# Performance work log

Hardware: AMD Instinct MI355X
Metric: run time of the kernel (lower is better)

The kernel has to match this reference:

```python
import jax, jax.numpy as jnp
import numpy as np


def setup_inputs() -> dict:
    key = jax.random.key(0)
    k1, k2, k3, k4 = jax.random.split(key, 4)
    B, S, H, P = 8, 2048, 1024, 4096
    hidden_states = jax.random.normal(k1, (B, S, H), dtype=jnp.float32)
    pairs = jax.random.randint(k2, (B, P, 2), 0, S, dtype=jnp.int64)
    # classifier params: Linear(2H -> H), Linear(H -> 2). Stored as (in, out).
    W1 = jax.random.normal(k3, (2 * H, H), dtype=jnp.float32) * (1.0 / np.sqrt(2 * H))
    b1 = jnp.zeros((H,), dtype=jnp.float32)
    W2 = jax.random.normal(k4, (H, 2), dtype=jnp.float32) * (1.0 / np.sqrt(H))
    b2 = jnp.zeros((2,), dtype=jnp.float32)
    return {"hidden_states": hidden_states, "pairs": pairs,
            "W1": W1, "b1": b1, "W2": W2, "b2": b2}


def reference(hidden_states, pairs, W1, b1, W2, b2):
    # Gather pair embeddings: (B, P, H) each.
    emb1 = jnp.take_along_axis(hidden_states, pairs[:, :, 0:1], axis=1)
    emb2 = jnp.take_along_axis(hidden_states, pairs[:, :, 1:2], axis=1)
    pair_emb = jnp.concatenate([emb1, emb2], axis=-1)  # (B, P, 2H)
    h = jnp.einsum('bpi,ih->bph', pair_emb, W1) + b1
    h = jax.nn.gelu(h, approximate=False)  # torch nn.GELU default is exact erf
    # Dropout is identity at inference.
    logits = jnp.einsum('bph,ho->bpo', h, W2) + b2  # (B, P, 2)
    return logits
```

## Files before the change

kernel.cpp:

```cpp
#include <hip/hip_runtime.h>
#include <hip/hip_bf16.h>

#define B_  8
#define S_  2048
#define H_  1024
#define P_  4096
#define K_  2048
#define M_  32768
#define NT_ 32

typedef unsigned short u16;
using bf16x8 = __attribute__((ext_vector_type(8))) short;
using f32x4  = __attribute__((ext_vector_type(4))) float;

#define AS1 __attribute__((address_space(1)))
#define AS3 __attribute__((address_space(3)))

__device__ inline u16 f2bf(float f) {
  union { float f; unsigned u; } c; c.f = f;
  unsigned u = c.u;
  unsigned r = (u + 0x7fffu + ((u >> 16) & 1u)) >> 16;
  return (u16)r;
}

__global__ void cvt_hidden_k(const float4* __restrict__ src,
                             ushort4* __restrict__ dst, int n4) {
  int i = blockIdx.x * blockDim.x + threadIdx.x;
  int stride = gridDim.x * blockDim.x;
  for (; i < n4; i += stride) {
    float4 v = src[i];
    ushort4 o;
    o.x = f2bf(v.x); o.y = f2bf(v.y); o.z = f2bf(v.z); o.w = f2bf(v.w);
    dst[i] = o;
  }
}

__global__ void transp_w1_k(const float* __restrict__ w1, u16* __restrict__ w1t) {
  __shared__ float tile[32][33];
  int n0 = blockIdx.x * 32;
  int k0 = blockIdx.y * 32;
  int tx = threadIdx.x;
  int ty = threadIdx.y;
#pragma unroll
  for (int i = 0; i < 32; i += 8)
    tile[ty + i][tx] = w1[(size_t)(k0 + ty + i) * H_ + n0 + tx];
  __syncthreads();
#pragma unroll
  for (int i = 0; i < 32; i += 8)
    w1t[(size_t)(n0 + ty + i) * K_ + k0 + tx] = f2bf(tile[tx][ty + i]);
}

__global__ __launch_bounds__(256, 2) void gemm_k(
    const u16*  __restrict__ hidB,
    const u16*  __restrict__ w1t,
    const int*  __restrict__ pairs,
    const float* __restrict__ b1,
    const float2* __restrict__ w2,
    float*      __restrict__ part)
{
  __shared__ u16 lds[2][16384];

  int orig = blockIdx.x;
  int bid = (orig & 7) * 256 + (orig >> 3);
  int nt = bid & 7;
  int mt = bid >> 3;
  int n0 = nt * 128;
  int m0 = mt * 128;
  int bI = m0 >> 12;
  int pp = m0 & 4095;

  int t = threadIdx.x;
  int w = t >> 6;
  int l = t & 63;
  int lr = l & 15;
  int lj = l >> 4;
  int wr = w >> 1;
  int wn = w & 1;

  int gsrc = (l & 7) ^ ((l >> 3) & 7);
  unsigned xo[2];
  xo[0] = (unsigned)(((lj) ^ (l & 7)) * 8);
  xo[1] = (unsigned)(((4 + lj) ^ (l & 7)) * 8);

  int2 sv[4];
#pragma unroll
  for (int i = 0; i < 4; ++i)
    sv[i] = ((const int2*)pairs)[bI * P_ + pp + i * 32 + (t >> 3)];

  const u16* hidBase = hidB + ((size_t)bI << 21);

  f32x4 acc[4][4];
#pragma unroll
  for (int i = 0; i < 4; ++i)
#pragma unroll
    for (int j = 0; j < 4; ++j)
      acc[i][j] = (f32x4){0.f, 0.f, 0.f, 0.f};

  auto STAGE = [&](int buf, int T) {
    int k0 = T * 64;
    int kcol = k0 & 1023;
    int half = k0 >> 10;
    unsigned dbase = (unsigned)buf * 16384u + (unsigned)t * 8u;
#pragma unroll
    for (int i = 0; i < 4; ++i) {
      int s = half ? sv[i].y : sv[i].x;
      __builtin_amdgcn_global_load_lds(
          (const AS1 void*)(hidBase + (((size_t)s) << 10) + kcol + gsrc * 8),
          (AS3 void*)&lds[0][dbase + (unsigned)i * 2048u], 16, 0, 0);
    }
    int r = t >> 3;
#pragma unroll
    for (int i = 0; i < 4; ++i) {
      __builtin_amdgcn_global_load_lds(
          (const AS1 void*)(w1t + (size_t)(n0 + i * 32 + r) * K_ + k0 + gsrc * 8),
          (AS3 void*)&lds[0][dbase + 8192u + (unsigned)i * 2048u], 16, 0, 0);
    }
  };

  STAGE(0, 0);
  __syncthreads();

  for (int T = 0; T < NT_; ++T) {
    int cur = T & 1;
    if (T + 1 < NT_) STAGE(cur ^ 1, T + 1);

    bf16x8 af[2][4], bv[2][4];
#pragma unroll
    for (int kk = 0; kk < 2; ++kk) {
#pragma unroll
      for (int mi = 0; mi < 4; ++mi)
        af[kk][mi] = *(const bf16x8*)&lds[cur][
            (unsigned)(wr * 64 + mi * 16 + lr) * 64u + xo[kk]];
#pragma unroll
      for (int ni = 0; ni < 4; ++ni)
        bv[kk][ni] = *(const bf16x8*)&lds[cur][8192u +
            (unsigned)(wn * 64 + ni * 16 + lr) * 64u + xo[kk]];
    }
    __builtin_amdgcn_s_setprio(1);
#pragma unroll
    for (int kk = 0; kk < 2; ++kk)
#pragma unroll
      for (int mi = 0; mi < 4; ++mi)
#pragma unroll
        for (int ni = 0; ni < 4; ++ni)
          acc[mi][ni] = __builtin_amdgcn_mfma_f32_16x16x32_bf16(
              af[kk][mi], bv[kk][ni], acc[mi][ni], 0, 0, 0);
    __builtin_amdgcn_s_setprio(0);
    __syncthreads();
  }

  int q = nt * 2 + wn;
  float2* pOut = (float2*)part;
#pragma unroll
  for (int mi = 0; mi < 4; ++mi) {
    float s0[4] = {0.f, 0.f, 0.f, 0.f};
    float s1[4] = {0.f, 0.f, 0.f, 0.f};
#pragma unroll
    for (int ni = 0; ni < 4; ++ni) {
      int n = n0 + wn * 64 + ni * 16 + lr;
      float bb = b1[n];
      float2 wv = w2[n];
#pragma unroll
      for (int j = 0; j < 4; ++j) {
        float x = acc[mi][ni][j] + bb;
        float g = 0.5f * x * (1.0f + erff(x * 0.70710678118654752f));
        s0[j] += g * wv.x;
        s1[j] += g * wv.y;
      }
    }
#pragma unroll
    for (int off = 1; off < 16; off <<= 1) {
#pragma unroll
      for (int j = 0; j < 4; ++j) {
        s0[j] += __shfl_xor(s0[j], off, 64);
        s1[j] += __shfl_xor(s1[j], off, 64);
      }
    }
    if (lr == 0) {
#pragma unroll
      for (int j = 0; j < 4; ++j) {
        int m = m0 + wr * 64 + mi * 16 + lj * 4 + j;
        pOut[((size_t)q << 15) + m] = make_float2(s0[j], s1[j]);
      }
    }
  }
}

__global__ void reduce_k(const float2* __restrict__ part,
                         const float* __restrict__ b2,
                         float2* __restrict__ out) {
  int m = blockIdx.x * blockDim.x + threadIdx.x;
  if (m >= M_) return;
  float a0 = b2[0], a1 = b2[1];
#pragma unroll
  for (int q = 0; q < 16; ++q) {
    float2 v = part[((size_t)q << 15) + m];
    a0 += v.x; a1 += v.y;
  }
  out[m] = make_float2(a0, a1);
}

extern "C" void kernel_launch(void* const* d_in, const int* in_sizes, int n_in,
                              void* d_out, int out_size, void* d_ws, size_t ws_size,
                              hipStream_t stream) {
  const float* hidden = (const float*)d_in[0];
  const int*   pairs  = (const int*)d_in[1];
  const float* W1     = (const float*)d_in[2];
  const float* b1     = (const float*)d_in[3];
  const float* W2     = (const float*)d_in[4];
  const float* b2     = (const float*)d_in[5];
  float* out = (float*)d_out;

  u16* hidB = (u16*)d_ws;
  u16* w1t  = hidB + (size_t)B_ * S_ * H_;
  float* part = (float*)(w1t + (size_t)H_ * K_);

  int n4 = (B_ * S_ * H_) / 4;
  cvt_hidden_k<<<4096, 256, 0, stream>>>((const float4*)hidden, (ushort4*)hidB, n4);
  transp_w1_k<<<dim3(H_ / 32, K_ / 32), dim3(32, 8), 0, stream>>>(W1, w1t);
  gemm_k<<<(M_ / 128) * (H_ / 128), 256, 0, stream>>>(
      hidB, w1t, pairs, b1, (const float2*)W2, part);
  reduce_k<<<(M_ + 255) / 256, 256, 0, stream>>>(
      (const float2*)part, b2, (float2*)out);
}
```

Baseline: 178.8 us.

## Project hidden states through W1 halves before gathering pairs

Splits W1 into its top and bottom halves and runs one GEMM over all sequence positions, with N=2048, instead of a GEMM over the gathered pair rows. Each pair's hidden pre-activation then comes from adding two gathered bf16 projection rows. A separate kernel does that addition, the bias, GELU and the W2 dot product per pair with a wave reduction. This roughly halves the matmul FLOPs because P·2 exceeds S. In exchange it writes a large bf16 intermediate and adds a gather read, rounds the partial sums to bf16 before they are added, and processes batches in chunks sized to the workspace.

```diff
diff --git a/kernel.cpp b/kernel.cpp
--- a/kernel.cpp
+++ b/kernel.cpp
@@ -5,9 +5,6 @@
 #define S_  2048
 #define H_  1024
 #define P_  4096
-#define K_  2048
-#define M_  32768
-#define NT_ 32
 
 typedef unsigned short u16;
 using bf16x8 = __attribute__((ext_vector_type(8))) short;
@@ -21,6 +18,10 @@
   unsigned u = c.u;
   unsigned r = (u + 0x7fffu + ((u >> 16) & 1u)) >> 16;
   return (u16)r;
+}
+__device__ inline float bf2f(u16 v) {
+  union { unsigned u; float f; } c; c.u = ((unsigned)v) << 16;
+  return c.f;
 }
 
 __global__ void cvt_hidden_k(const float4* __restrict__ src,
@@ -35,39 +36,38 @@
   }
 }
 
-__global__ void transp_w1_k(const float* __restrict__ w1, u16* __restrict__ w1t) {
+__global__ void transp_w1_k(const float* __restrict__ w1, u16* __restrict__ bT) {
   __shared__ float tile[32][33];
   int n0 = blockIdx.x * 32;
   int k0 = blockIdx.y * 32;
+  int srcR = (n0 >> 10) * 1024 + k0;
+  int srcC = n0 & 1023;
   int tx = threadIdx.x;
   int ty = threadIdx.y;
 #pragma unroll
   for (int i = 0; i < 32; i += 8)
-    tile[ty + i][tx] = w1[(size_t)(k0 + ty + i) * H_ + n0 + tx];
+    tile[ty + i][tx] = w1[(size_t)(srcR + ty + i) * H_ + srcC + tx];
   __syncthreads();
 #pragma unroll
   for (int i = 0; i < 32; i += 8)
-    w1t[(size_t)(n0 + ty + i) * K_ + k0 + tx] = f2bf(tile[tx][ty + i]);
+    bT[(size_t)(n0 + ty + i) * 1024 + k0 + tx] = f2bf(tile[tx][ty + i]);
 }
 
 __global__ __launch_bounds__(256, 2) void gemm_k(
-    const u16*  __restrict__ hidB,
-    const u16*  __restrict__ w1t,
-    const int*  __restrict__ pairs,
-    const float* __restrict__ b1,
-    const float2* __restrict__ w2,
-    float*      __restrict__ part)
+    const u16* __restrict__ A,
+    const u16* __restrict__ bT,
+    u16*       __restrict__ C,
+    int mtiles)
 {
-  __shared__ u16 lds[2][16384];
-
+  __shared__ u16 lds[2 * 16384];
+
+  int nblocks = mtiles * 16;
   int orig = blockIdx.x;
-  int bid = (orig & 7) * 256 + (orig >> 3);
-  int nt = bid & 7;
-  int mt = bid >> 3;
+  int bid = (orig & 7) * (nblocks >> 3) + (orig >> 3);
+  int nt = bid & 15;
+  int mt = bid >> 4;
   int n0 = nt * 128;
   int m0 = mt * 128;
-  int bI = m0 >> 12;
-  int pp = m0 & 4095;
 
   int t = threadIdx.x;
   int w = t >> 6;
@@ -82,12 +82,8 @@
   xo[0] = (unsigned)(((lj) ^ (l & 7)) * 8);
   xo[1] = (unsigned)(((4 + lj) ^ (l & 7)) * 8);
 
-  int2 sv[4];
-#pragma unroll
-  for (int i = 0; i < 4; ++i)
-    sv[i] = ((const int2*)pairs)[bI * P_ + pp + i * 32 + (t >> 3)];
-
-  const u16* hidBase = hidB + ((size_t)bI << 21);
+  const u16* aBase = A  + (size_t)m0 * 1024;
+  const u16* bBase = bT + (size_t)n0 * 1024;
 
   f32x4 acc[4][4];
 #pragma unroll
@@ -98,42 +94,37 @@
 
   auto STAGE = [&](int buf, int T) {
     int k0 = T * 64;
-    int kcol = k0 & 1023;
-    int half = k0 >> 10;
     unsigned dbase = (unsigned)buf * 16384u + (unsigned)t * 8u;
-#pragma unroll
-    for (int i = 0; i < 4; ++i) {
-      int s = half ? sv[i].y : sv[i].x;
+    int r = t >> 3;
+#pragma unroll
+    for (int i = 0; i < 4; ++i)
       __builtin_amdgcn_global_load_lds(
-          (const AS1 void*)(hidBase + (((size_t)s) << 10) + kcol + gsrc * 8),
-          (AS3 void*)&lds[0][dbase + (unsigned)i * 2048u], 16, 0, 0);
-    }
-    int r = t >> 3;
-#pragma unroll
-    for (int i = 0; i < 4; ++i) {
+          (const AS1 void*)(aBase + (size_t)(i * 32 + r) * 1024 + k0 + gsrc * 8),
+          (AS3 void*)&lds[dbase + (unsigned)i * 2048u], 16, 0, 0);
+#pragma unroll
+    for (int i = 0; i < 4; ++i)
       __builtin_amdgcn_global_load_lds(
-          (const AS1 void*)(w1t + (size_t)(n0 + i * 32 + r) * K_ + k0 + gsrc * 8),
-          (AS3 void*)&lds[0][dbase + 8192u + (unsigned)i * 2048u], 16, 0, 0);
-    }
+          (const AS1 void*)(bBase + (size_t)(i * 32 + r) * 1024 + k0 + gsrc * 8),
+          (AS3 void*)&lds[dbase + 8192u + (unsigned)i * 2048u], 16, 0, 0);
   };
 
   STAGE(0, 0);
   __syncthreads();
 
-  for (int T = 0; T < NT_; ++T) {
+  for (int T = 0; T < 16; ++T) {
     int cur = T & 1;
-    if (T + 1 < NT_) STAGE(cur ^ 1, T + 1);
+    if (T + 1 < 16) STAGE(cur ^ 1, T + 1);
 
     bf16x8 af[2][4], bv[2][4];
 #pragma unroll
     for (int kk = 0; kk < 2; ++kk) {
 #pragma unroll
       for (int mi = 0; mi < 4; ++mi)
-        af[kk][mi] = *(const bf16x8*)&lds[cur][
+        af[kk][mi] = *(const bf16x8*)&lds[(unsigned)cur * 16384u +
             (unsigned)(wr * 64 + mi * 16 + lr) * 64u + xo[kk]];
 #pragma unroll
       for (int ni = 0; ni < 4; ++ni)
-        bv[kk][ni] = *(const bf16x8*)&lds[cur][8192u +
+        bv[kk][ni] = *(const bf16x8*)&lds[(unsigned)cur * 16384u + 8192u +
             (unsigned)(wn * 64 + ni * 16 + lr) * 64u + xo[kk]];
     }
     __builtin_amdgcn_s_setprio(1);
@@ -149,55 +140,61 @@
     __syncthreads();
   }
 
-  int q = nt * 2 + wn;
-  float2* pOut = (float2*)part;
-#pragma unroll
-  for (int mi = 0; mi < 4; ++mi) {
-    float s0[4] = {0.f, 0.f, 0.f, 0.f};
-    float s1[4] = {0.f, 0.f, 0.f, 0.f};
-#pragma unroll
-    for (int ni = 0; ni < 4; ++ni) {
-      int n = n0 + wn * 64 + ni * 16 + lr;
-      float bb = b1[n];
-      float2 wv = w2[n];
-#pragma unroll
-      for (int j = 0; j < 4; ++j) {
-        float x = acc[mi][ni][j] + bb;
-        float g = 0.5f * x * (1.0f + erff(x * 0.70710678118654752f));
-        s0[j] += g * wv.x;
-        s1[j] += g * wv.y;
-      }
-    }
-#pragma unroll
-    for (int off = 1; off < 16; off <<= 1) {
-#pragma unroll
-      for (int j = 0; j < 4; ++j) {
-        s0[j] += __shfl_xor(s0[j], off, 64);
-        s1[j] += __shfl_xor(s1[j], off, 64);
-      }
-    }
-    if (lr == 0) {
-#pragma unroll
-      for (int j = 0; j < 4; ++j) {
-        int m = m0 + wr * 64 + mi * 16 + lj * 4 + j;
-        pOut[((size_t)q << 15) + m] = make_float2(s0[j], s1[j]);
-      }
-    }
-  }
-}
-
-__global__ void reduce_k(const float2* __restrict__ part,
-                         const float* __restrict__ b2,
-                         float2* __restrict__ out) {
-  int m = blockIdx.x * blockDim.x + threadIdx.x;
-  if (m >= M_) return;
-  float a0 = b2[0], a1 = b2[1];
-#pragma unroll
-  for (int q = 0; q < 16; ++q) {
-    float2 v = part[((size_t)q << 15) + m];
-    a0 += v.x; a1 += v.y;
-  }
-  out[m] = make_float2(a0, a1);
+#pragma unroll
+  for (int mi = 0; mi < 4; ++mi)
+#pragma unroll
+    for (int ni = 0; ni < 4; ++ni)
+#pragma unroll
+      for (int j = 0; j < 4; ++j)
+        C[(size_t)(m0 + wr * 64 + mi * 16 + lj * 4 + j) * 2048 +
+          (n0 + wn * 64 + ni * 16 + lr)] = f2bf(acc[mi][ni][j]);
+}
+
+__global__ __launch_bounds__(256) void gelu_w2_k(
+    const u16* __restrict__ C,
+    const int* __restrict__ pairs,
+    const float* __restrict__ b1,
+    const float2* __restrict__ w2,
+    const float* __restrict__ b2,
+    float2* __restrict__ out,
+    int b0, int nb)
+{
+  int nblocks = nb * 1024;
+  int orig = blockIdx.x;
+  int bid = (orig & 7) * (nblocks >> 3) + (orig >> 3);
+  int w = threadIdx.x >> 6;
+  int l = threadIdx.x & 63;
+  int pr = bid * 4 + w;
+  int bL = pr >> 12;
+  int p  = pr & 4095;
+  int2 sv = ((const int2*)pairs)[(size_t)(b0 + bL) * P_ + p];
+
+  const u16* Ub = C + (((size_t)(bL * 2048 + sv.x)) << 11) + l * 16;
+  const u16* Vb = C + (((size_t)(bL * 2048 + sv.y)) << 11) + 1024 + l * 16;
+  bf16x8 u0 = *(const bf16x8*)Ub;
+  bf16x8 u1 = *(const bf16x8*)(Ub + 8);
+  bf16x8 v0 = *(const bf16x8*)Vb;
+  bf16x8 v1 = *(const bf16x8*)(Vb + 8);
+
+  int n = l * 16;
+  float o0 = 0.f, o1 = 0.f;
+#pragma unroll
+  for (int e = 0; e < 16; ++e) {
+    u16 ue = (u16)(e < 8 ? u0[e] : u1[e - 8]);
+    u16 ve = (u16)(e < 8 ? v0[e] : v1[e - 8]);
+    float h = bf2f(ue) + bf2f(ve) + b1[n + e];
+    float g = 0.5f * h * (1.0f + erff(h * 0.70710678118654752f));
+    float2 wv = w2[n + e];
+    o0 += g * wv.x;
+    o1 += g * wv.y;
+  }
+#pragma unroll
+  for (int off = 1; off < 64; off <<= 1) {
+    o0 += __shfl_xor(o0, off, 64);
+    o1 += __shfl_xor(o1, off, 64);
+  }
+  if (l == 0)
+    out[(size_t)(b0 + bL) * P_ + p] = make_float2(o0 + b2[0], o1 + b2[1]);
 }
 
 extern "C" void kernel_launch(void* const* d_in, const int* in_sizes, int n_in,
@@ -211,15 +208,26 @@
   const float* b2     = (const float*)d_in[5];
   float* out = (float*)d_out;
 
-  u16* hidB = (u16*)d_ws;
-  u16* w1t  = hidB + (size_t)B_ * S_ * H_;
-  float* part = (float*)(w1t + (size_t)H_ * K_);
-
-  int n4 = (B_ * S_ * H_) / 4;
-  cvt_hidden_k<<<4096, 256, 0, stream>>>((const float4*)hidden, (ushort4*)hidB, n4);
-  transp_w1_k<<<dim3(H_ / 32, K_ / 32), dim3(32, 8), 0, stream>>>(W1, w1t);
-  gemm_k<<<(M_ / 128) * (H_ / 128), 256, 0, stream>>>(
-      hidB, w1t, pairs, b1, (const float2*)W2, part);
-  reduce_k<<<(M_ + 255) / 256, 256, 0, stream>>>(
-      (const float2*)part, b2, (float2*)out);
-}
+  const size_t MB = 1u << 20;
+  int nb = 8;
+  while (nb > 1 && ws_size < 4 * MB + (size_t)nb * 12 * MB) nb >>= 1;
+  int np = 8 / nb;
+
+  u16* bT   = (u16*)d_ws;
+  u16* hidB = bT + (size_t)2048 * 1024;
+  u16* C    = hidB + (size_t)nb * 2048 * 1024;
+
+  transp_w1_k<<<dim3(2048 / 32, 1024 / 32), dim3(32, 8), 0, stream>>>(W1, bT);
+
+  for (int ps = 0; ps < np; ++ps) {
+    int b0 = ps * nb;
+    int n4 = nb * 2048 * 1024 / 4;
+    cvt_hidden_k<<<2048, 256, 0, stream>>>(
+        (const float4*)(hidden + (size_t)b0 * 2048 * 1024),
+        (ushort4*)hidB, n4);
+    int mtiles = nb * 16;
+    gemm_k<<<mtiles * 16, 256, 0, stream>>>(hidB, bT, C, mtiles);
+    gelu_w2_k<<<nb * 1024, 256, 0, stream>>>(
+        C, pairs, b1, (const float2*)W2, b2, (float2*)out, b0, nb);
+  }
+}
```

Measured after the change: 209.2 us. 1.17x slower.
